# Kernel optimization log

Measured on AMD Instinct MI355X. Metric: run time of the kernel, lower is better.

Reference implementation:

```python
import jax, jax.numpy as jnp
import numpy as np

B, N1, N2, DIM = 16, 1024, 4096, 512
EPS_BN = 1e-5   # torch BatchNorm1d default eps
EPS_FP = 1e-8   # PointNet++ FP inverse-distance eps


def setup_inputs() -> dict:
    key = jax.random.key(0)
    ks = jax.random.split(key, 6)
    s1 = 1.0 / np.sqrt(2 * DIM)
    s2 = 1.0 / np.sqrt(DIM)
    return {
        "xyz1": jax.random.normal(ks[0], (B, N1, 3), jnp.float32),
        "points1": jax.random.normal(ks[1], (B, N1, 2 * DIM), jnp.float32),
        "xyz2": jax.random.normal(ks[2], (B, N2, 3), jnp.float32),
        "points2": jax.random.normal(ks[3], (B, N2, DIM), jnp.float32),
        "fc1_w": jax.random.normal(ks[4], (2 * DIM, DIM), jnp.float32) * s1,
        "fc1_b": jnp.zeros((DIM,), jnp.float32),
        "bn1_gamma": jnp.ones((DIM,), jnp.float32),
        "bn1_beta": jnp.zeros((DIM,), jnp.float32),
        "fc2_w": jax.random.normal(ks[5], (DIM, DIM), jnp.float32) * s2,
        "fc2_b": jnp.zeros((DIM,), jnp.float32),
        "bn2_gamma": jnp.ones((DIM,), jnp.float32),
        "bn2_beta": jnp.zeros((DIM,), jnp.float32),
    }


def _bn_relu(x, gamma, beta):
    # BatchNorm1d (training mode, batch stats) over (B, L) per channel; x is [B, L, C]
    mu = jnp.mean(x, axis=(0, 1), keepdims=True)
    var = jnp.var(x, axis=(0, 1), keepdims=True)
    return jax.nn.relu((x - mu) * jax.lax.rsqrt(var + EPS_BN) * gamma + beta)


def _fp_interpolate(xyz_dst, xyz_src, feats_src):
    # PointNet++ inverse-distance 3-NN interpolation.
    # xyz_dst [B,N,3], xyz_src [B,S,3], feats_src [B,S,C] -> [B,N,C]
    d = (jnp.sum(xyz_dst * xyz_dst, -1)[:, :, None]
         + jnp.sum(xyz_src * xyz_src, -1)[:, None, :]
         - 2.0 * jnp.einsum('bnd,bsd->bns', xyz_dst, xyz_src))  # squared dists [B,N,S]
    neg_d3, idx3 = jax.lax.top_k(-d, 3)                          # 3 smallest dists
    w = 1.0 / (-neg_d3 + EPS_FP)                                  # [B,N,3]
    w = w / jnp.sum(w, -1, keepdims=True)
    # gather: [B,1,S,C] indexed along axis 2 by [B,N,3,1] -> [B,N,3,C]
    gathered = jnp.take_along_axis(feats_src[:, None, :, :], idx3[..., None], axis=2)
    return jnp.einsum('bnkc,bnk->bnc', gathered, w)


def reference(xyz1, points1, xyz2, points2,
              fc1_w, fc1_b, bn1_gamma, bn1_beta,
              fc2_w, fc2_b, bn2_gamma, bn2_beta):
    feats1 = _bn_relu(points1 @ fc1_w + fc1_b, bn1_gamma, bn1_beta)   # [B,N1,DIM]
    feats1 = _fp_interpolate(xyz2, xyz1, feats1)                      # [B,N2,DIM]
    feats2 = _bn_relu(points2 @ fc2_w + fc2_b, bn2_gamma, bn2_beta)   # [B,N2,DIM]
    return (xyz2, feats1 + feats2)
```

## Files before the change

### kernel.cpp

```cpp
#include <hip/hip_runtime.h>
#include <stdint.h>

typedef unsigned short u16;
typedef __attribute__((ext_vector_type(8))) short short8;
typedef __attribute__((ext_vector_type(4))) float floatx4;

#define BB 16
#define NN1 1024
#define NN2 4096
#define DIM 512
#define M1 (BB*NN1)
#define M2 (BB*NN2)

__device__ __forceinline__ float bf2f(u16 u){
  union { unsigned int i; float f; } v; v.i = ((unsigned int)u) << 16; return v.f;
}
__device__ __forceinline__ u16 f2bf(float f){
  union { float f; unsigned int i; } v; v.f = f;
  unsigned int i = v.i;
  return (u16)((i + 0x7FFFu + ((i >> 16) & 1u)) >> 16);
}

__device__ __forceinline__ uint32_t cvtpk(float lo, float hi){
  uint32_t r;
  asm("v_cvt_pk_bf16_f32 %0, %1, %2" : "=v"(r) : "v"(lo), "v"(hi));
  return r;
}

__device__ __forceinline__ float rcpf(float x){
  float r; asm("v_rcp_f32 %0, %1" : "=v"(r) : "v"(x)); return r;
}

__device__ __forceinline__ void gload_lds16(const void* g, void* l){
  __builtin_amdgcn_global_load_lds(
      (const __attribute__((address_space(1))) void*)g,
      (__attribute__((address_space(3))) void*)l, 16, 0, 0);
}

__global__ void prep(const float* __restrict__ fc1_w, const float* __restrict__ fc2_w,
                     u16* __restrict__ wT1, u16* __restrict__ wT2,
                     float* __restrict__ stats){
  int idx = blockIdx.x * 256 + threadIdx.x;
  if (idx < 2048) stats[idx] = 0.0f;
  if (idx < 512 * 1024){
    int n = idx >> 10, k = idx & 1023;
    wT1[idx] = f2bf(fc1_w[k * 512 + n]);
  } else {
    int j = idx - 512 * 1024;
    int n = j >> 9, k = j & 511;
    wT2[j] = f2bf(fc2_w[k * 512 + n]);
  }
}

__global__ __launch_bounds__(256) void gemm_mfma(
    const float* __restrict__ A, const u16* __restrict__ BT,
    const float* __restrict__ bias, void* __restrict__ Yv,
    int M, int K, int out_is_f32,
    float* __restrict__ sum, float* __restrict__ sumsq)
{
  const int N = 512;
  __shared__ u16 As[2][128 * 32];
  __shared__ u16 Bs[2][128 * 32];
  int tid  = threadIdx.x;
  int lane = tid & 63, wave = tid >> 6;

  int id = blockIdx.x;
  int bm = (id & 7) + ((id >> 5) << 3);
  int bn = (id >> 3) & 3;

  int wm = (wave & 1) * 64, wn = (wave >> 1) * 64;
  int r16 = lane & 15, quad = lane >> 4;

  floatx4 acc[4][4];
#pragma unroll
  for (int i = 0; i < 4; i++)
#pragma unroll
    for (int j = 0; j < 4; j++)
      acc[i][j] = (floatx4)(0.0f);

  int lr = tid >> 2;
  int kc = tid & 3;

  const float* Ag = A  + (size_t)(bm * 128) * K;
  const u16*   Bg = BT + (size_t)(bn * 128) * K;

  const float* ap0 = Ag + (size_t)lr * K + kc * 8;
  const float* ap1 = Ag + (size_t)(lr + 64) * K + kc * 8;
  int adst0 = lr * 32 + ((kc ^ ((lr >> 1) & 3)) * 8);
  int adst1 = adst0 + 64 * 32;

  int pb0 = wave * 128 + lane;
  int rb0 = pb0 >> 2, cb0 = (pb0 & 3) ^ ((rb0 >> 1) & 3);
  int pb1 = pb0 + 64;
  int rb1 = pb1 >> 2, cb1 = (pb1 & 3) ^ ((rb1 >> 1) & 3);
  const u16* bsrc0 = Bg + (size_t)rb0 * K + cb0 * 8;
  const u16* bsrc1 = Bg + (size_t)rb1 * K + cb1 * 8;
  int boff = (wave * 128) * 8;

  int rsw = ((r16 >> 1) & 3) ^ quad;

  int NS = K >> 5;
  float4 a00, a01, a10, a11;

  a00 = *(const float4*)(ap0);     a01 = *(const float4*)(ap0 + 4);
  a10 = *(const float4*)(ap1);     a11 = *(const float4*)(ap1 + 4);
  gload_lds16(bsrc0, &Bs[0][boff]);
  gload_lds16(bsrc1, &Bs[0][boff + 512]);
  {
    uint4 tv0, tv1;
    tv0.x = cvtpk(a00.x, a00.y); tv0.y = cvtpk(a00.z, a00.w);
    tv0.z = cvtpk(a01.x, a01.y); tv0.w = cvtpk(a01.z, a01.w);
    tv1.x = cvtpk(a10.x, a10.y); tv1.y = cvtpk(a10.z, a10.w);
    tv1.z = cvtpk(a11.x, a11.y); tv1.w = cvtpk(a11.z, a11.w);
    *(uint4*)(&As[0][adst0]) = tv0;
    *(uint4*)(&As[0][adst1]) = tv1;
  }
  __syncthreads();

  int cur = 0;
  for (int ks = 0; ks < NS; ks++){
    int k1 = (ks + 1) << 5;
    if (ks + 1 < NS){
      a00 = *(const float4*)(ap0 + k1); a01 = *(const float4*)(ap0 + k1 + 4);
      a10 = *(const float4*)(ap1 + k1); a11 = *(const float4*)(ap1 + k1 + 4);
      gload_lds16(bsrc0 + k1, &Bs[cur ^ 1][boff]);
      gload_lds16(bsrc1 + k1, &Bs[cur ^ 1][boff + 512]);
    }
    short8 af[4], bfr[4];
#pragma unroll
    for (int i = 0; i < 4; i++) af[i]  = *(const short8*)(&As[cur][(wm + i*16 + r16) * 32 + rsw * 8]);
#pragma unroll
    for (int j = 0; j < 4; j++) bfr[j] = *(const short8*)(&Bs[cur][(wn + j*16 + r16) * 32 + rsw * 8]);
#pragma unroll
    for (int i = 0; i < 4; i++)
#pragma unroll
      for (int j = 0; j < 4; j++)
        acc[i][j] = __builtin_amdgcn_mfma_f32_16x16x32_bf16(af[i], bfr[j], acc[i][j], 0, 0, 0);
    if (ks + 1 < NS){
      uint4 tv0, tv1;
      tv0.x = cvtpk(a00.x, a00.y); tv0.y = cvtpk(a00.z, a00.w);
      tv0.z = cvtpk(a01.x, a01.y); tv0.w = cvtpk(a01.z, a01.w);
      tv1.x = cvtpk(a10.x, a10.y); tv1.y = cvtpk(a10.z, a10.w);
      tv1.z = cvtpk(a11.x, a11.y); tv1.w = cvtpk(a11.z, a11.w);
      *(uint4*)(&As[cur ^ 1][adst0]) = tv0;
      *(uint4*)(&As[cur ^ 1][adst1]) = tv1;
    }
    __syncthreads();
    cur ^= 1;
  }

  float cs[4] = {0.f, 0.f, 0.f, 0.f};
  float cq[4] = {0.f, 0.f, 0.f, 0.f};
#pragma unroll
  for (int i = 0; i < 4; i++){
    int rowb = bm * 128 + wm + i * 16 + quad * 4;
#pragma unroll
    for (int j = 0; j < 4; j++){
      int col = bn * 128 + wn + j * 16 + r16;
      float bv = bias[col];
#pragma unroll
      for (int r = 0; r < 4; r++){
        float v = acc[i][j][r] + bv;
        cs[j] += v; cq[j] += v * v;
        size_t idx = (size_t)(rowb + r) * N + col;
        if (out_is_f32) ((float*)Yv)[idx] = v;
        else            ((u16*)Yv)[idx]   = f2bf(v);
      }
    }
  }

#pragma unroll
  for (int j = 0; j < 4; j++){
    cs[j] += __shfl_xor(cs[j], 16); cs[j] += __shfl_xor(cs[j], 32);
    cq[j] += __shfl_xor(cq[j], 16); cq[j] += __shfl_xor(cq[j], 32);
  }
  float* S = (float*)As;
  if (lane < 16){
    int wmh = wave & 1, wnh = wave >> 1;
#pragma unroll
    for (int j = 0; j < 4; j++){
      int c = wnh * 64 + j * 16 + r16;
      S[wmh * 256 + c]       = cs[j];
      S[wmh * 256 + 128 + c] = cq[j];
    }
  }
  __syncthreads();
  {
    int stat = tid >> 7, c = tid & 127;
    float v = S[stat * 128 + c] + S[256 + stat * 128 + c];
    float* dstp = stat ? sumsq : sum;
    atomicAdd(&dstp[bn * 128 + c], v);
  }
}

__global__ void bn_coeff_copy(const float* __restrict__ stats,
                              const float* __restrict__ g1, const float* __restrict__ be1,
                              const float* __restrict__ g2, const float* __restrict__ be2,
                              float* __restrict__ coef,
                              const uint4* __restrict__ xsrc, uint4* __restrict__ xdst){
  int b = blockIdx.x, tid = threadIdx.x;
  if (b == 0){
    int c = tid;
    {
      float mu  = stats[c] / (float)M1;
      float var = stats[512 + c] / (float)M1 - mu * mu;
      var = fmaxf(var, 0.0f);
      float a = g1[c] * (1.0f / sqrtf(var + 1e-5f));
      coef[c] = a;
      coef[512 + c] = be1[c] - mu * a;
    }
    {
      float mu  = stats[1024 + c] / (float)M2;
      float var = stats[1536 + c] / (float)M2 - mu * mu;
      var = fmaxf(var, 0.0f);
      float a = g2[c] * (1.0f / sqrtf(var + 1e-5f));
      coef[1024 + c] = a;
      coef[1536 + c] = be2[c] - mu * a;
    }
  } else {
    int i = (b - 1) * 512 + tid;
    xdst[i] = xsrc[i];
  }
}

__global__ __launch_bounds__(64) void interp_final(
    const float* __restrict__ xyz1, const float* __restrict__ xyz2,
    const u16* __restrict__ Y1, const float* __restrict__ coef,
    float* __restrict__ outF)
{
  int lane = threadIdx.x;
  int bid  = blockIdx.x;
  int b = bid >> 12;

  const float* pd = xyz2 + (size_t)bid * 3;
  double xd = (double)pd[0];
  double yd = (double)pd[1];
  double zd = (double)pd[2];

  unsigned long long kl[16];
  const float* ps = xyz1 + (size_t)b * NN1 * 3;
#pragma unroll
  for (int s = 0; s < 16; s++){
    const float* q = ps + (s * 64 + lane) * 3;
    double dx = xd - (double)q[0];
    double dy = yd - (double)q[1];
    double dz = zd - (double)q[2];
    double d = dx * dx + dy * dy + dz * dz;
    unsigned long long bits = (unsigned long long)__double_as_longlong(d);
    kl[s] = (bits & ~1023ULL) | (unsigned long long)(s * 64 + lane);
  }

  unsigned long long selk[3];
  for (int p = 0; p < 3; p++){
    unsigned long long m = kl[0];
#pragma unroll
    for (int s = 1; s < 16; s++) if (kl[s] < m) m = kl[s];
    for (int off = 1; off < 64; off <<= 1){
      unsigned long long o = (unsigned long long)__shfl_xor((long long)m, off);
      if (o < m) m = o;
    }
    selk[p] = m;
    if (p < 2){
#pragma unroll
      for (int s = 0; s < 16; s++) if (kl[s] == m) kl[s] = ~0ULL;
    }
  }

  int i0 = (int)(selk[0] & 1023ULL);
  int i1 = (int)(selk[1] & 1023ULL);
  int i2 = (int)(selk[2] & 1023ULL);
  float d0 = (float)__longlong_as_double((long long)(selk[0] & ~1023ULL));
  float d1 = (float)__longlong_as_double((long long)(selk[1] & ~1023ULL));
  float d2 = (float)__longlong_as_double((long long)(selk[2] & ~1023ULL));
  float w0 = rcpf(d0 + 1e-8f);
  float w1 = rcpf(d1 + 1e-8f);
  float w2 = rcpf(d2 + 1e-8f);
  float inv = rcpf(w0 + w1 + w2);
  float f0 = w0 * inv, f1 = w1 * inv, f2 = w2 * inv;

  const u16* r0 = Y1 + (size_t)(b * NN1 + i0) * DIM;
  const u16* r1 = Y1 + (size_t)(b * NN1 + i1) * DIM;
  const u16* r2 = Y1 + (size_t)(b * NN1 + i2) * DIM;
  float* o = outF + (size_t)bid * DIM;

  int c0 = lane * 8;
  uint4 q0 = *(const uint4*)(r0 + c0);
  uint4 q1 = *(const uint4*)(r1 + c0);
  uint4 q2 = *(const uint4*)(r2 + c0);
  float4 ylo = *(const float4*)(o + c0);
  float4 yhi = *(const float4*)(o + c0 + 4);
  union { float4 v[2]; float f[8]; } A1u, B1u, A2u, B2u;
  A1u.v[0] = *(const float4*)(coef + c0);        A1u.v[1] = *(const float4*)(coef + c0 + 4);
  B1u.v[0] = *(const float4*)(coef + 512 + c0);  B1u.v[1] = *(const float4*)(coef + 512 + c0 + 4);
  A2u.v[0] = *(const float4*)(coef + 1024 + c0); A2u.v[1] = *(const float4*)(coef + 1024 + c0 + 4);
  B2u.v[0] = *(const float4*)(coef + 1536 + c0); B2u.v[1] = *(const float4*)(coef + 1536 + c0 + 4);
  const u16* p0 = (const u16*)&q0;
  const u16* p1 = (const u16*)&q1;
  const u16* p2 = (const u16*)&q2;
  float yv[8] = { ylo.x, ylo.y, ylo.z, ylo.w, yhi.x, yhi.y, yhi.z, yhi.w };
  float res[8];
#pragma unroll
  for (int j = 0; j < 8; j++){
    float a1 = A1u.f[j], b1 = B1u.f[j];
    float a2 = A2u.f[j], b2 = B2u.f[j];
    float v0 = fmaxf(a1 * bf2f(p0[j]) + b1, 0.0f);
    float v1 = fmaxf(a1 * bf2f(p1[j]) + b1, 0.0f);
    float v2 = fmaxf(a1 * bf2f(p2[j]) + b1, 0.0f);
    float vi = f0 * v0 + f1 * v1 + f2 * v2;
    float y2 = fmaxf(a2 * yv[j] + b2, 0.0f);
    res[j] = vi + y2;
  }
  *(float4*)(o + c0)     = make_float4(res[0], res[1], res[2], res[3]);
  *(float4*)(o + c0 + 4) = make_float4(res[4], res[5], res[6], res[7]);
}

extern "C" void kernel_launch(void* const* d_in, const int* in_sizes, int n_in,
                              void* d_out, int out_size, void* d_ws, size_t ws_size,
                              hipStream_t stream){
  const float* xyz1    = (const float*)d_in[0];
  const float* points1 = (const float*)d_in[1];
  const float* xyz2    = (const float*)d_in[2];
  const float* points2 = (const float*)d_in[3];
  const float* fc1_w   = (const float*)d_in[4];
  const float* fc1_b   = (const float*)d_in[5];
  const float* bn1_g   = (const float*)d_in[6];
  const float* bn1_b   = (const float*)d_in[7];
  const float* fc2_w   = (const float*)d_in[8];
  const float* fc2_b   = (const float*)d_in[9];
  const float* bn2_g   = (const float*)d_in[10];
  const float* bn2_b   = (const float*)d_in[11];

  char* ws = (char*)d_ws;
  u16*   Y1    = (u16*)(ws);
  u16*   wT1   = (u16*)(ws + 16777216);
  u16*   wT2   = (u16*)(ws + 17825792);
  float* stats = (float*)(ws + 18350080);
  float* coef  = (float*)(ws + 18358272);

  float* out  = (float*)d_out;
  float* outF = out + 196608;

  prep<<<3072, 256, 0, stream>>>(fc1_w, fc2_w, wT1, wT2, stats);

  gemm_mfma<<<512, 256, 0, stream>>>(points1, wT1, fc1_b, Y1,   M1, 1024, 0,
                                     stats,        stats + 512);
  gemm_mfma<<<2048, 256, 0, stream>>>(points2, wT2, fc2_b, outF, M2,  512, 1,
                                      stats + 1024, stats + 1536);

  bn_coeff_copy<<<97, 512, 0, stream>>>(stats, bn1_g, bn1_b, bn2_g, bn2_b, coef,
                                        (const uint4*)xyz2, (uint4*)out);

  interp_final<<<65536, 64, 0, stream>>>(xyz1, xyz2, Y1, coef, outF);
}
```

Baseline: 462.1 us.

## Use fp32 kNN distances with fp64 fallback on ties; widen GEMM to 512 threads

The interpolation kernel now computes squared distances in fp32 and packs distance bits with the index into a 64-bit key. It selects four nearest candidates and recomputes in fp64 only when the third and fourth distances are nearly tied, so tie ordering stays correct while the common path avoids costly double arithmetic. The GEMM kernel moves to 512 threads per block, with each wave covering a 64x32 output sub-tile and each thread loading half as much data. That gives more waves for latency hiding at the cost of lower per-wave register reuse. The extra fourth selection pass adds some reduction work in the fast path.

Measured after the change: 481.7 us. 1.04x slower.

```diff
diff --git a/kernel.cpp b/kernel.cpp
--- a/kernel.cpp
+++ b/kernel.cpp
@@ -52,7 +52,7 @@
   }
 }
 
-__global__ __launch_bounds__(256) void gemm_mfma(
+__global__ __launch_bounds__(512, 4) void gemm_mfma(
     const float* __restrict__ A, const u16* __restrict__ BT,
     const float* __restrict__ bias, void* __restrict__ Yv,
     int M, int K, int out_is_f32,
@@ -68,52 +68,41 @@
   int bm = (id & 7) + ((id >> 5) << 3);
   int bn = (id >> 3) & 3;
 
-  int wm = (wave & 1) * 64, wn = (wave >> 1) * 64;
+  int wm = (wave & 1) * 64, wn = (wave >> 1) * 32;
   int r16 = lane & 15, quad = lane >> 4;
 
-  floatx4 acc[4][4];
+  floatx4 acc[4][2];
 #pragma unroll
   for (int i = 0; i < 4; i++)
 #pragma unroll
-    for (int j = 0; j < 4; j++)
+    for (int j = 0; j < 2; j++)
       acc[i][j] = (floatx4)(0.0f);
-
-  int lr = tid >> 2;
-  int kc = tid & 3;
 
   const float* Ag = A  + (size_t)(bm * 128) * K;
   const u16*   Bg = BT + (size_t)(bn * 128) * K;
 
-  const float* ap0 = Ag + (size_t)lr * K + kc * 8;
-  const float* ap1 = Ag + (size_t)(lr + 64) * K + kc * 8;
-  int adst0 = lr * 32 + ((kc ^ ((lr >> 1) & 3)) * 8);
-  int adst1 = adst0 + 64 * 32;
-
-  int pb0 = wave * 128 + lane;
-  int rb0 = pb0 >> 2, cb0 = (pb0 & 3) ^ ((rb0 >> 1) & 3);
-  int pb1 = pb0 + 64;
-  int rb1 = pb1 >> 2, cb1 = (pb1 & 3) ^ ((rb1 >> 1) & 3);
-  const u16* bsrc0 = Bg + (size_t)rb0 * K + cb0 * 8;
-  const u16* bsrc1 = Bg + (size_t)rb1 * K + cb1 * 8;
-  int boff = (wave * 128) * 8;
+  int ar  = tid >> 2;
+  int akc = tid & 3;
+  const float* ap = Ag + (size_t)ar * K + akc * 8;
+  int adst = ar * 32 + ((akc ^ ((ar >> 1) & 3)) * 8);
+
+  int brow = tid >> 2, bpos = tid & 3;
+  int bkc  = bpos ^ ((brow >> 1) & 3);
+  const u16* bsrc = Bg + (size_t)brow * K + bkc * 8;
+  int bdoff = tid * 8;
 
   int rsw = ((r16 >> 1) & 3) ^ quad;
 
   int NS = K >> 5;
-  float4 a00, a01, a10, a11;
-
-  a00 = *(const float4*)(ap0);     a01 = *(const float4*)(ap0 + 4);
-  a10 = *(const float4*)(ap1);     a11 = *(const float4*)(ap1 + 4);
-  gload_lds16(bsrc0, &Bs[0][boff]);
-  gload_lds16(bsrc1, &Bs[0][boff + 512]);
+  float4 a0, a1;
+
+  a0 = *(const float4*)(ap);  a1 = *(const float4*)(ap + 4);
+  gload_lds16(bsrc, &Bs[0][bdoff]);
   {
-    uint4 tv0, tv1;
-    tv0.x = cvtpk(a00.x, a00.y); tv0.y = cvtpk(a00.z, a00.w);
-    tv0.z = cvtpk(a01.x, a01.y); tv0.w = cvtpk(a01.z, a01.w);
-    tv1.x = cvtpk(a10.x, a10.y); tv1.y = cvtpk(a10.z, a10.w);
-    tv1.z = cvtpk(a11.x, a11.y); tv1.w = cvtpk(a11.z, a11.w);
-    *(uint4*)(&As[0][adst0]) = tv0;
-    *(uint4*)(&As[0][adst1]) = tv1;
+    uint4 tv;
+    tv.x = cvtpk(a0.x, a0.y); tv.y = cvtpk(a0.z, a0.w);
+    tv.z = cvtpk(a1.x, a1.y); tv.w = cvtpk(a1.z, a1.w);
+    *(uint4*)(&As[0][adst]) = tv;
   }
   __syncthreads();
 
@@ -121,41 +110,36 @@
   for (int ks = 0; ks < NS; ks++){
     int k1 = (ks + 1) << 5;
     if (ks + 1 < NS){
-      a00 = *(const float4*)(ap0 + k1); a01 = *(const float4*)(ap0 + k1 + 4);
-      a10 = *(const float4*)(ap1 + k1); a11 = *(const float4*)(ap1 + k1 + 4);
-      gload_lds16(bsrc0 + k1, &Bs[cur ^ 1][boff]);
-      gload_lds16(bsrc1 + k1, &Bs[cur ^ 1][boff + 512]);
-    }
-    short8 af[4], bfr[4];
+      a0 = *(const float4*)(ap + k1);  a1 = *(const float4*)(ap + k1 + 4);
+      gload_lds16(bsrc + k1, &Bs[cur ^ 1][bdoff]);
+    }
+    short8 af[4], bfr[2];
 #pragma unroll
     for (int i = 0; i < 4; i++) af[i]  = *(const short8*)(&As[cur][(wm + i*16 + r16) * 32 + rsw * 8]);
 #pragma unroll
-    for (int j = 0; j < 4; j++) bfr[j] = *(const short8*)(&Bs[cur][(wn + j*16 + r16) * 32 + rsw * 8]);
+    for (int j = 0; j < 2; j++) bfr[j] = *(const short8*)(&Bs[cur][(wn + j*16 + r16) * 32 + rsw * 8]);
 #pragma unroll
     for (int i = 0; i < 4; i++)
 #pragma unroll
-      for (int j = 0; j < 4; j++)
+      for (int j = 0; j < 2; j++)
         acc[i][j] = __builtin_amdgcn_mfma_f32_16x16x32_bf16(af[i], bfr[j], acc[i][j], 0, 0, 0);
     if (ks + 1 < NS){
-      uint4 tv0, tv1;
-      tv0.x = cvtpk(a00.x, a00.y); tv0.y = cvtpk(a00.z, a00.w);
-      tv0.z = cvtpk(a01.x, a01.y); tv0.w = cvtpk(a01.z, a01.w);
-      tv1.x = cvtpk(a10.x, a10.y); tv1.y = cvtpk(a10.z, a10.w);
-      tv1.z = cvtpk(a11.x, a11.y); tv1.w = cvtpk(a11.z, a11.w);
-      *(uint4*)(&As[cur ^ 1][adst0]) = tv0;
-      *(uint4*)(&As[cur ^ 1][adst1]) = tv1;
+      uint4 tv;
+      tv.x = cvtpk(a0.x, a0.y); tv.y = cvtpk(a0.z, a0.w);
+      tv.z = cvtpk(a1.x, a1.y); tv.w = cvtpk(a1.z, a1.w);
+      *(uint4*)(&As[cur ^ 1][adst]) = tv;
     }
     __syncthreads();
     cur ^= 1;
   }
 
-  float cs[4] = {0.f, 0.f, 0.f, 0.f};
-  float cq[4] = {0.f, 0.f, 0.f, 0.f};
+  float cs[2] = {0.f, 0.f};
+  float cq[2] = {0.f, 0.f};
 #pragma unroll
   for (int i = 0; i < 4; i++){
     int rowb = bm * 128 + wm + i * 16 + quad * 4;
 #pragma unroll
-    for (int j = 0; j < 4; j++){
+    for (int j = 0; j < 2; j++){
       int col = bn * 128 + wn + j * 16 + r16;
       float bv = bias[col];
 #pragma unroll
@@ -170,22 +154,22 @@
   }
 
 #pragma unroll
-  for (int j = 0; j < 4; j++){
+  for (int j = 0; j < 2; j++){
     cs[j] += __shfl_xor(cs[j], 16); cs[j] += __shfl_xor(cs[j], 32);
     cq[j] += __shfl_xor(cq[j], 16); cq[j] += __shfl_xor(cq[j], 32);
   }
   float* S = (float*)As;
   if (lane < 16){
-    int wmh = wave & 1, wnh = wave >> 1;
-#pragma unroll
-    for (int j = 0; j < 4; j++){
-      int c = wnh * 64 + j * 16 + r16;
+    int wmh = wave & 1;
+#pragma unroll
+    for (int j = 0; j < 2; j++){
+      int c = wn + j * 16 + r16;
       S[wmh * 256 + c]       = cs[j];
       S[wmh * 256 + 128 + c] = cq[j];
     }
   }
   __syncthreads();
-  {
+  if (tid < 256){
     int stat = tid >> 7, c = tid & 127;
     float v = S[stat * 128 + c] + S[256 + stat * 128 + c];
     float* dstp = stat ? sumsq : sum;
@@ -233,25 +217,22 @@
   int b = bid >> 12;
 
   const float* pd = xyz2 + (size_t)bid * 3;
-  double xd = (double)pd[0];
-  double yd = (double)pd[1];
-  double zd = (double)pd[2];
+  float xf = pd[0], yf = pd[1], zf = pd[2];
+  const float* ps = xyz1 + (size_t)b * NN1 * 3;
 
   unsigned long long kl[16];
-  const float* ps = xyz1 + (size_t)b * NN1 * 3;
 #pragma unroll
   for (int s = 0; s < 16; s++){
     const float* q = ps + (s * 64 + lane) * 3;
-    double dx = xd - (double)q[0];
-    double dy = yd - (double)q[1];
-    double dz = zd - (double)q[2];
-    double d = dx * dx + dy * dy + dz * dz;
-    unsigned long long bits = (unsigned long long)__double_as_longlong(d);
-    kl[s] = (bits & ~1023ULL) | (unsigned long long)(s * 64 + lane);
-  }
-
-  unsigned long long selk[3];
-  for (int p = 0; p < 3; p++){
+    float dx = xf - q[0], dy = yf - q[1], dz = zf - q[2];
+    float d = fmaf(dx, dx, fmaf(dy, dy, dz * dz));
+    kl[s] = ((unsigned long long)__float_as_uint(d) << 32)
+          | (unsigned int)(s * 64 + lane);
+  }
+
+  unsigned long long selk[4];
+#pragma unroll
+  for (int p = 0; p < 4; p++){
     unsigned long long m = kl[0];
 #pragma unroll
     for (int s = 1; s < 16; s++) if (kl[s] < m) m = kl[s];
@@ -260,23 +241,68 @@
       if (o < m) m = o;
     }
     selk[p] = m;
-    if (p < 2){
+    if (p < 3){
 #pragma unroll
       for (int s = 0; s < 16; s++) if (kl[s] == m) kl[s] = ~0ULL;
     }
   }
 
-  int i0 = (int)(selk[0] & 1023ULL);
-  int i1 = (int)(selk[1] & 1023ULL);
-  int i2 = (int)(selk[2] & 1023ULL);
-  float d0 = (float)__longlong_as_double((long long)(selk[0] & ~1023ULL));
-  float d1 = (float)__longlong_as_double((long long)(selk[1] & ~1023ULL));
-  float d2 = (float)__longlong_as_double((long long)(selk[2] & ~1023ULL));
-  float w0 = rcpf(d0 + 1e-8f);
-  float w1 = rcpf(d1 + 1e-8f);
-  float w2 = rcpf(d2 + 1e-8f);
-  float inv = rcpf(w0 + w1 + w2);
-  float f0 = w0 * inv, f1 = w1 * inv, f2 = w2 * inv;
+  float d3 = __uint_as_float((unsigned int)(selk[2] >> 32));
+  float d4 = __uint_as_float((unsigned int)(selk[3] >> 32));
+
+  int i0, i1, i2;
+  float f0, f1, f2;
+  if (d4 - d3 > (d4 + d3) * 7.62939453125e-6f){
+    i0 = (int)(selk[0] & 0xFFFFFFFFULL);
+    i1 = (int)(selk[1] & 0xFFFFFFFFULL);
+    i2 = (int)(selk[2] & 0xFFFFFFFFULL);
+    float e0 = __uint_as_float((unsigned int)(selk[0] >> 32));
+    float e1 = __uint_as_float((unsigned int)(selk[1] >> 32));
+    float w0 = rcpf(e0 + 1e-8f);
+    float w1 = rcpf(e1 + 1e-8f);
+    float w2 = rcpf(d3 + 1e-8f);
+    float inv = rcpf(w0 + w1 + w2);
+    f0 = w0 * inv; f1 = w1 * inv; f2 = w2 * inv;
+  } else {
+    double xd = (double)xf, yd = (double)yf, zd = (double)zf;
+#pragma unroll
+    for (int s = 0; s < 16; s++){
+      const float* q = ps + (s * 64 + lane) * 3;
+      double dx = xd - (double)q[0];
+      double dy = yd - (double)q[1];
+      double dz = zd - (double)q[2];
+      double d = dx * dx + dy * dy + dz * dz;
+      unsigned long long bits = (unsigned long long)__double_as_longlong(d);
+      kl[s] = (bits & ~1023ULL) | (unsigned long long)(s * 64 + lane);
+    }
+    unsigned long long sel2[3];
+#pragma unroll
+    for (int p = 0; p < 3; p++){
+      unsigned long long m = kl[0];
+#pragma unroll
+      for (int s = 1; s < 16; s++) if (kl[s] < m) m = kl[s];
+      for (int off = 1; off < 64; off <<= 1){
+        unsigned long long o = (unsigned long long)__shfl_xor((long long)m, off);
+        if (o < m) m = o;
+      }
+      sel2[p] = m;
+      if (p < 2){
+#pragma unroll
+        for (int s = 0; s < 16; s++) if (kl[s] == m) kl[s] = ~0ULL;
+      }
+    }
+    i0 = (int)(sel2[0] & 1023ULL);
+    i1 = (int)(sel2[1] & 1023ULL);
+    i2 = (int)(sel2[2] & 1023ULL);
+    float e0 = (float)__longlong_as_double((long long)(sel2[0] & ~1023ULL));
+    float e1 = (float)__longlong_as_double((long long)(sel2[1] & ~1023ULL));
+    float e2 = (float)__longlong_as_double((long long)(sel2[2] & ~1023ULL));
+    float w0 = rcpf(e0 + 1e-8f);
+    float w1 = rcpf(e1 + 1e-8f);
+    float w2 = rcpf(e2 + 1e-8f);
+    float inv = rcpf(w0 + w1 + w2);
+    f0 = w0 * inv; f1 = w1 * inv; f2 = w2 * inv;
+  }
 
   const u16* r0 = Y1 + (size_t)(b * NN1 + i0) * DIM;
   const u16* r1 = Y1 + (size_t)(b * NN1 + i1) * DIM;
@@ -342,9 +368,9 @@
 
   prep<<<3072, 256, 0, stream>>>(fc1_w, fc2_w, wT1, wT2, stats);
 
-  gemm_mfma<<<512, 256, 0, stream>>>(points1, wT1, fc1_b, Y1,   M1, 1024, 0,
+  gemm_mfma<<<512, 512, 0, stream>>>(points1, wT1, fc1_b, Y1,   M1, 1024, 0,
                                      stats,        stats + 512);
-  gemm_mfma<<<2048, 256, 0, stream>>>(points2, wT2, fc2_b, outF, M2,  512, 1,
+  gemm_mfma<<<2048, 512, 0, stream>>>(points2, wT2, fc2_b, outF, M2,  512, 1,
                                       stats + 1024, stats + 1536);
 
   bn_coeff_copy<<<97, 512, 0, stream>>>(stats, bn1_g, bn1_b, bn2_g, bn2_b, coef,
```
